# Performance work log

Hardware: AMD Instinct MI355X
Metric: run time of the kernel (lower is better)

The kernel has to match this reference:

```python
import jax, jax.numpy as jnp
import numpy as np

GRID = 32


def setup_inputs() -> dict:
    key = jax.random.key(0)
    k1, k2, k3 = jax.random.split(key, 3)
    # points in [-0.5, 0.5] per the module's asserts
    x = jax.random.uniform(k1, (8, 3, 50000), minval=-0.5, maxval=0.5, dtype=jnp.float32)
    # prep = Conv2d(3, 16, kernel_size=1): weight [C,3], bias [C]
    W = jax.random.normal(k2, (16, 3), dtype=jnp.float32) * 0.1
    bias = jax.random.normal(k3, (16,), dtype=jnp.float32) * 0.1
    return {"x": x, "W": W, "bias": bias}


def reference(x, W, bias):
    G = GRID
    b, _, n = x.shape
    reshaped = (x + 0.5) * G - 0.5                      # [b,3,n]
    ind1 = jnp.clip(jnp.floor(reshaped), 0.0, G - 1)
    ind2 = jnp.clip(jnp.ceil(reshaped), 0.0, G - 1)
    # 8 corners, ordered (floor/ceil over x, then y, then z) to match original list
    corners = []
    for cx in (ind1, ind2):
        for cy in (ind1, ind2):
            for cz in (ind1, ind2):
                corners.append(jnp.stack([cx[:, 0], cy[:, 1], cz[:, 2]], axis=1))
    ind = jnp.stack(corners, axis=-1)                   # [b,3,n,8]
    res = reshaped[..., None] - ind                     # [b,3,n,8] residuals
    flat_idx = (ind[:, 0] * (G * G) + ind[:, 1] * G + ind[:, 2]).astype(jnp.int32)  # [b,n,8]
    flat_idx = jnp.clip(flat_idx, 0, G ** 3)            # mirrors indices.clamp_(0, G**3)
    dist = jnp.linalg.norm(res, axis=1)                 # [b,n,8]
    weight = (dist < 0.87).astype(res.dtype)            # [b,n,8] (detached in original)
    # prep: 1x1 conv over channel dim
    feat = jnp.einsum('bknp,ck->bcnp', res, W) + bias[None, :, None, None]  # [b,c,n,8]
    feat = feat * weight[:, None]                       # mask by ball weight
    c = feat.shape[1]
    feat_f = feat.reshape(b, c, n * 8)
    w_f = jnp.broadcast_to(weight[:, None], feat.shape).reshape(b, c, n * 8)
    i_f = flat_idx.reshape(b, n * 8)

    def scatter_one(f, w, idx):
        g = jnp.zeros((c, G ** 3), f.dtype).at[:, idx].add(f)
        cnt = jnp.zeros((c, G ** 3), f.dtype).at[:, idx].add(w)
        return g, cnt

    grid, count = jax.vmap(scatter_one)(feat_f, w_f, i_f)  # [b,c,G^3] each
    grid = grid / jnp.maximum(count, 1.0)
    return grid.reshape(b, c, G, G, G)
```

## Files before the change

### kernel.cpp

```cpp
#include <hip/hip_runtime.h>

#define G 32
#define G2 (G*G)
#define G3 (G*G*G)
#define NPTS 50000
#define NB 8
#define NC 16
#define NCHUNK_PER_B 49
#define NCHUNK (NB*NCHUNK_PER_B)
#define SUBCAP 1024

#define OFF_HIST    0
#define OFF_PAYLOAD 65536


__global__ __launch_bounds__(1024) void ge_bin(const float* __restrict__ x,
                                               int* __restrict__ hist,
                                               unsigned long long* __restrict__ payload) {
    __shared__ unsigned long long sp[2048];
    __shared__ unsigned char spl[2048];
    __shared__ int h[G];
    __shared__ int offs[G + 1];

    const int tid = threadIdx.x;
    const int b   = blockIdx.y;
    const int c   = b * NCHUNK_PER_B + blockIdx.x;
    const int n   = blockIdx.x * 1024 + tid;
    const bool valid = n < NPTS;

    if (tid < G) h[tid] = 0;
    __syncthreads();

    unsigned long long e1 = 0, e2 = 0;
    int p1 = 0, p2 = 0, r1 = 0, r2 = 0;
    bool put1 = false, put2 = false;

    if (valid) {
        const float* xb = x + (size_t)b * 3 * NPTS;
        float rx = (xb[n]          + 0.5f) * 32.0f - 0.5f;
        float ry = (xb[NPTS + n]   + 0.5f) * 32.0f - 0.5f;
        float rz = (xb[2*NPTS + n] + 0.5f) * 32.0f - 0.5f;
        p1 = (int)fminf(fmaxf(floorf(rx), 0.0f), 31.0f);
        p2 = (int)fminf(fmaxf(ceilf (rx), 0.0f), 31.0f);

        float fy1 = fminf(fmaxf(floorf(ry), 0.0f), 31.0f);
        float fy2 = fminf(fmaxf(ceilf (ry), 0.0f), 31.0f);
        float fz1 = fminf(fmaxf(floorf(rz), 0.0f), 31.0f);
        float fz2 = fminf(fmaxf(ceilf (rz), 0.0f), 31.0f);
        float dy1 = ry - fy1, dy2 = ry - fy2;
        float dz1 = rz - fz1, dz2 = rz - fz2;
        float dy1s = dy1 * dy1, dy2s = dy2 * dy2;
        float dz1s = dz1 * dz1, dz2s = dz2 * dz2;

        int iy1 = (int)fy1, sy = (int)fy2 - iy1;
        int iz1 = (int)fz1, sz = (int)fz2 - iz1;
        int ay1 = (int)rintf(dy1 * 2048.0f) + 2048;
        int az1 = (int)rintf(dz1 * 2048.0f) + 2048;
        unsigned long long common =
              ((unsigned long long)(unsigned)ay1 << 30)
            | ((unsigned long long)(unsigned)az1 << 17)
            | ((unsigned long long)(unsigned)iy1 << 12)
            | ((unsigned long long)(unsigned)iz1 << 7)
            | ((unsigned long long)(unsigned)sy  << 6)
            | ((unsigned long long)(unsigned)sz  << 5);
        unsigned fr1 = (p1 == p2) ? 2u : 1u;

        {
            float dx = rx - (float)p1;
            float dx2 = dx * dx;
            float a0 = dx2 + dy1s, a1 = dx2 + dy2s;
            unsigned m = 0;
            if (a0 + dz1s < 0.7569f) m |= 1u;
            if (a0 + dz2s < 0.7569f) m |= 2u;
            if (a1 + dz1s < 0.7569f) m |= 4u;
            if (a1 + dz2s < 0.7569f) m |= 8u;
            if (m) {
                unsigned ax = (unsigned)((int)rintf(dx * 2048.0f) + 2048);
                e1 = ((unsigned long long)ax << 43) | common
                   | ((unsigned long long)(fr1 - 1u) << 4) | m;
                put1 = true;
                r1 = atomicAdd(&h[p1], 1);
            }
        }
        if (p2 != p1) {
            float dx = rx - (float)p2;
            float dx2 = dx * dx;
            float a0 = dx2 + dy1s, a1 = dx2 + dy2s;
            unsigned m = 0;
            if (a0 + dz1s < 0.7569f) m |= 1u;
            if (a0 + dz2s < 0.7569f) m |= 2u;
            if (a1 + dz1s < 0.7569f) m |= 4u;
            if (a1 + dz2s < 0.7569f) m |= 8u;
            if (m) {
                unsigned ax = (unsigned)((int)rintf(dx * 2048.0f) + 2048);
                e2 = ((unsigned long long)ax << 43) | common | m;
                put2 = true;
                r2 = atomicAdd(&h[p2], 1);
            }
        }
    }
    __syncthreads();

    if (tid == 0) {
        int run = 0;
        #pragma unroll
        for (int p = 0; p < G; ++p) { offs[p] = run; run += h[p]; }
        offs[G] = run;
    }
    __syncthreads();

    if (put1) {
        int i1 = offs[p1] + r1;
        sp[i1] = e1; spl[i1] = (unsigned char)p1;
    }
    if (put2) {
        int i2 = offs[p2] + r2;
        sp[i2] = e2; spl[i2] = (unsigned char)p2;
    }
    if (tid < G) hist[c * G + tid] = h[tid];
    __syncthreads();

    const int T = offs[G];
    unsigned long long* chunk_pl = payload + (size_t)c * G * SUBCAP;
    for (int e = tid; e < T; e += 1024) {
        int p = spl[e];
        chunk_pl[(size_t)p * SUBCAP + (e - offs[p])] = sp[e];
    }
}

__global__ __launch_bounds__(1024) void ge_accum(const unsigned long long* __restrict__ payload,
                                                 const int* __restrict__ hist,
                                                 const float* __restrict__ W,
                                                 const float* __restrict__ bias,
                                                 float* __restrict__ out) {
    __shared__ unsigned long long A[G2];
    const int tid = threadIdx.x;
    const int b = blockIdx.x >> 5;
    const int s = blockIdx.x & 31;

    A[tid] = 0ull;
    __syncthreads();

    const int wave = tid >> 6, lane = tid & 63;
    for (int blk = wave; blk < NCHUNK_PER_B; blk += 16) {
        const int cc = b * NCHUNK_PER_B + blk;
        const int ec = hist[cc * G + s];
        const unsigned long long* q = payload + ((size_t)cc * G + s) * SUBCAP;
        for (int i = lane; i < ec; i += 64) {
            unsigned long long e = q[i];
            unsigned m   = (unsigned)e & 15u;
            unsigned fr  = 1u + (((unsigned)e >> 4) & 1u);
            int sz  = ((int)e >> 5) & 1;
            int sy  = ((int)e >> 6) & 1;
            int iz1 = ((int)e >> 7) & 31;
            int iy1 = ((int)e >> 12) & 31;
            unsigned az1 = (unsigned)(e >> 17) & 0x1FFFu;
            unsigned ay1 = (unsigned)(e >> 30) & 0x1FFFu;
            unsigned ax  = (unsigned)(e >> 43) & 0x1FFFu;

            unsigned long long base = ((unsigned long long)fr << 57)
                                    | ((unsigned long long)(ax * fr) << 38);
            unsigned ayl = ay1 * fr, ayh = (ay1 - 2048u * sy) * fr;
            unsigned azl = az1 * fr, azh = (az1 - 2048u * sz) * fr;
            int cell = iy1 * G + iz1;

            if (m & 1u) atomicAdd(&A[cell],
                ((unsigned long long)ayl << 19) | azl | base);
            if (m & 2u) atomicAdd(&A[cell + sz],
                ((unsigned long long)ayl << 19) | azh | base);
            if (m & 4u) atomicAdd(&A[cell + G * sy],
                ((unsigned long long)ayh << 19) | azl | base);
            if (m & 8u) atomicAdd(&A[cell + G * sy + sz],
                ((unsigned long long)ayh << 19) | azh | base);
        }
    }
    __syncthreads();

    const unsigned long long a = A[tid];
    const float cw  = (float)(unsigned)(a >> 57);
    const float fxs = (float)(unsigned)((a >> 38) & 0x7FFFFull);
    const float fys = (float)(unsigned)((a >> 19) & 0x7FFFFull);
    const float fzs = (float)(unsigned)( a         & 0x7FFFFull);
    const float kq = 1.0f / 2048.0f;
    const float sx = (fxs - 2048.0f * cw) * kq;
    const float sy = (fys - 2048.0f * cw) * kq;
    const float sz = (fzs - 2048.0f * cw) * kq;
    const float inv = 1.0f / fmaxf(cw, 1.0f);

    float* ob = out + (size_t)b * NC * G3 + (size_t)s * G2 + tid;
    #pragma unroll
    for (int ch = 0; ch < NC; ++ch) {
        float v = W[ch * 3 + 0] * sx + W[ch * 3 + 1] * sy + W[ch * 3 + 2] * sz
                + cw * bias[ch];
        ob[(size_t)ch * G3] = v * inv;
    }
}

#define SEG 12288
#define QMAX SEG
__global__ __launch_bounds__(1024) void ge_fused(const float* __restrict__ x,
                                                 const float* __restrict__ W,
                                                 const float* __restrict__ bias,
                                                 float* __restrict__ out) {
    __shared__ float acc[G2][4];
    __shared__ int   q[QMAX];
    __shared__ int   qcount;
    const int b = blockIdx.x >> 5;
    const int s = blockIdx.x & 31;
    const float fs = (float)s;
    const int lane = threadIdx.x & 63;
    for (int i = threadIdx.x; i < G2 * 4; i += 1024) ((float*)acc)[i] = 0.0f;
    if (threadIdx.x == 0) qcount = 0;
    __syncthreads();
    const float* xb = x + (size_t)b * 3 * NPTS;
    for (int seg = 0; seg < NPTS; seg += SEG) {
        const int seg_end = (seg + SEG < NPTS) ? seg + SEG : NPTS;
        for (int base = seg; base < seg_end; base += 1024) {
            int n = base + threadIdx.x;
            bool pred = false; int tag = 0;
            if (n < seg_end) {
                float rx = (xb[n] + 0.5f) * 32.0f - 0.5f;
                int p1 = (int)fminf(fmaxf(floorf(rx), 0.0f), 31.0f);
                int p2 = (int)fminf(fmaxf(ceilf (rx), 0.0f), 31.0f);
                int reps = (p1 == s) + (p2 == s);
                pred = reps > 0;
                tag = n | (reps == 2 ? (int)0x80000000 : 0);
            }
            unsigned long long mask = __ballot(pred);
            int wcnt = __popcll(mask);
            if (wcnt) {
                int wbase = 0;
                if (lane == 0) wbase = atomicAdd(&qcount, wcnt);
                wbase = __shfl(wbase, 0);
                if (pred) q[wbase + __popcll(mask & ((1ULL << lane) - 1ULL))] = tag;
            }
        }
        __syncthreads();
        const int cnt = qcount;
        for (int i = threadIdx.x; i < cnt; i += 1024) {
            int e = q[i];
            int n = e & 0x7fffffff;
            float fr = (e < 0) ? 2.0f : 1.0f;
            float rx = (xb[n]          + 0.5f) * 32.0f - 0.5f;
            float ry = (xb[NPTS + n]   + 0.5f) * 32.0f - 0.5f;
            float rz = (xb[2*NPTS + n] + 0.5f) * 32.0f - 0.5f;
            float dx = rx - fs;
            float fy1 = fminf(fmaxf(floorf(ry), 0.0f), 31.0f);
            float fy2 = fminf(fmaxf(ceilf (ry), 0.0f), 31.0f);
            float fz1 = fminf(fmaxf(floorf(rz), 0.0f), 31.0f);
            float fz2 = fminf(fmaxf(ceilf (rz), 0.0f), 31.0f);
            #pragma unroll
            for (int cy = 0; cy < 2; ++cy) {
                float iy = cy ? fy2 : fy1;
                float dy = ry - iy;
                #pragma unroll
                for (int cz = 0; cz < 2; ++cz) {
                    float iz = cz ? fz2 : fz1;
                    float dz = rz - iz;
                    float d2 = dx * dx + dy * dy + dz * dz;
                    if (d2 < 0.7569f) {
                        int cell = (int)iy * G + (int)iz;
                        atomicAdd(&acc[cell][0], fr * dx);
                        atomicAdd(&acc[cell][1], fr * dy);
                        atomicAdd(&acc[cell][2], fr * dz);
                        atomicAdd(&acc[cell][3], fr);
                    }
                }
            }
        }
        __syncthreads();
        if (threadIdx.x == 0) qcount = 0;
        __syncthreads();
    }
    int cell = threadIdx.x;
    float sx = acc[cell][0], sy = acc[cell][1], sz = acc[cell][2], cnt = acc[cell][3];
    float inv = 1.0f / fmaxf(cnt, 1.0f);
    float* ob = out + (size_t)b * NC * G3 + (size_t)s * G2 + cell;
    #pragma unroll
    for (int c = 0; c < NC; ++c) {
        float v = W[c * 3 + 0] * sx + W[c * 3 + 1] * sy + W[c * 3 + 2] * sz
                + cnt * bias[c];
        ob[(size_t)c * G3] = v * inv;
    }
}

extern "C" void kernel_launch(void* const* d_in, const int* in_sizes, int n_in,
                              void* d_out, int out_size, void* d_ws, size_t ws_size,
                              hipStream_t stream) {
    const float* x    = (const float*)d_in[0];
    const float* W    = (const float*)d_in[1];
    const float* bias = (const float*)d_in[2];
    float* out = (float*)d_out;

    const size_t need = OFF_PAYLOAD
                      + (size_t)NCHUNK * G * SUBCAP * sizeof(unsigned long long);
    if (ws_size >= need) {
        char* wsb = (char*)d_ws;
        int* hist = (int*)(wsb + OFF_HIST);
        unsigned long long* payload = (unsigned long long*)(wsb + OFF_PAYLOAD);

        ge_bin  <<<dim3(NCHUNK_PER_B, NB), 1024, 0, stream>>>(x, hist, payload);
        ge_accum<<<NB * G, 1024, 0, stream>>>(payload, hist, W, bias, out);
    } else {
        ge_fused<<<NB * G, 1024, 0, stream>>>(x, W, bias, out);
    }
}
```

Baseline: 19.24 us.

## Compact per-bin payload via global atomic heads instead of per-chunk sub-buckets

Each binning block now reserves space in a single contiguous per-(batch, x-slice) bucket with one global atomicAdd per slice, replacing the per-chunk fixed-capacity sub-buckets and histogram. The accumulate kernel then streams one dense list per bin with all 1024 threads, instead of walking 49 sparse sub-lists per wave. Binning blocks shrink from 1024 to 256 threads to give more blocks. The change adds a memset launch and global atomics, and entries past a fixed capacity are silently dropped.

After: 25.52 us. 32.7% more time.

```diff
diff --git a/kernel.cpp b/kernel.cpp
--- a/kernel.cpp
+++ b/kernel.cpp
@@ -6,26 +6,26 @@
 #define NPTS 50000
 #define NB 8
 #define NC 16
-#define NCHUNK_PER_B 49
-#define NCHUNK (NB*NCHUNK_PER_B)
-#define SUBCAP 1024
-
-#define OFF_HIST    0
-#define OFF_PAYLOAD 65536
-
-
-__global__ __launch_bounds__(1024) void ge_bin(const float* __restrict__ x,
-                                               int* __restrict__ hist,
-                                               unsigned long long* __restrict__ payload) {
-    __shared__ unsigned long long sp[2048];
-    __shared__ unsigned char spl[2048];
+#define CHUNK 256
+#define NCHUNK_PER_B 196
+#define CAP 16384
+
+#define OFF_HEAD    0
+#define OFF_PAYLOAD 4096
+
+
+__global__ __launch_bounds__(256) void ge_bin(const float* __restrict__ x,
+                                              int* __restrict__ head,
+                                              unsigned long long* __restrict__ payload) {
+    __shared__ unsigned long long sp[2 * CHUNK];
+    __shared__ unsigned char spl[2 * CHUNK];
     __shared__ int h[G];
     __shared__ int offs[G + 1];
+    __shared__ int gbase[G];
 
     const int tid = threadIdx.x;
     const int b   = blockIdx.y;
-    const int c   = b * NCHUNK_PER_B + blockIdx.x;
-    const int n   = blockIdx.x * 1024 + tid;
+    const int n   = blockIdx.x * CHUNK + tid;
     const bool valid = n < NPTS;
 
     if (tid < G) h[tid] = 0;
@@ -109,70 +109,67 @@
     }
     __syncthreads();
 
-    if (put1) {
-        int i1 = offs[p1] + r1;
-        sp[i1] = e1; spl[i1] = (unsigned char)p1;
-    }
-    if (put2) {
-        int i2 = offs[p2] + r2;
-        sp[i2] = e2; spl[i2] = (unsigned char)p2;
-    }
-    if (tid < G) hist[c * G + tid] = h[tid];
+    if (tid < G) {
+        int c = h[tid];
+        gbase[tid] = c ? atomicAdd(&head[b * G + tid], c) : 0;
+    }
+    if (put1) { int i1 = offs[p1] + r1; sp[i1] = e1; spl[i1] = (unsigned char)p1; }
+    if (put2) { int i2 = offs[p2] + r2; sp[i2] = e2; spl[i2] = (unsigned char)p2; }
     __syncthreads();
 
     const int T = offs[G];
-    unsigned long long* chunk_pl = payload + (size_t)c * G * SUBCAP;
-    for (int e = tid; e < T; e += 1024) {
+    unsigned long long* pb = payload;
+    for (int e = tid; e < T; e += CHUNK) {
         int p = spl[e];
-        chunk_pl[(size_t)p * SUBCAP + (e - offs[p])] = sp[e];
+        size_t pos = (size_t)gbase[p] + (e - offs[p]);
+        if (pos < CAP)
+            pb[((size_t)b * G + p) * CAP + pos] = sp[e];
     }
 }
 
 __global__ __launch_bounds__(1024) void ge_accum(const unsigned long long* __restrict__ payload,
-                                                 const int* __restrict__ hist,
+                                                 const int* __restrict__ head,
                                                  const float* __restrict__ W,
                                                  const float* __restrict__ bias,
                                                  float* __restrict__ out) {
     __shared__ unsigned long long A[G2];
     const int tid = threadIdx.x;
-    const int b = blockIdx.x >> 5;
-    const int s = blockIdx.x & 31;
+    const int bin = blockIdx.x;
+    const int b = bin >> 5, s = bin & 31;
 
     A[tid] = 0ull;
     __syncthreads();
 
-    const int wave = tid >> 6, lane = tid & 63;
-    for (int blk = wave; blk < NCHUNK_PER_B; blk += 16) {
-        const int cc = b * NCHUNK_PER_B + blk;
-        const int ec = hist[cc * G + s];
-        const unsigned long long* q = payload + ((size_t)cc * G + s) * SUBCAP;
-        for (int i = lane; i < ec; i += 64) {
-            unsigned long long e = q[i];
-            unsigned m   = (unsigned)e & 15u;
-            unsigned fr  = 1u + (((unsigned)e >> 4) & 1u);
-            int sz  = ((int)e >> 5) & 1;
-            int sy  = ((int)e >> 6) & 1;
-            int iz1 = ((int)e >> 7) & 31;
-            int iy1 = ((int)e >> 12) & 31;
-            unsigned az1 = (unsigned)(e >> 17) & 0x1FFFu;
-            unsigned ay1 = (unsigned)(e >> 30) & 0x1FFFu;
-            unsigned ax  = (unsigned)(e >> 43) & 0x1FFFu;
-
-            unsigned long long base = ((unsigned long long)fr << 57)
-                                    | ((unsigned long long)(ax * fr) << 38);
-            unsigned ayl = ay1 * fr, ayh = (ay1 - 2048u * sy) * fr;
-            unsigned azl = az1 * fr, azh = (az1 - 2048u * sz) * fr;
-            int cell = iy1 * G + iz1;
-
-            if (m & 1u) atomicAdd(&A[cell],
-                ((unsigned long long)ayl << 19) | azl | base);
-            if (m & 2u) atomicAdd(&A[cell + sz],
-                ((unsigned long long)ayl << 19) | azh | base);
-            if (m & 4u) atomicAdd(&A[cell + G * sy],
-                ((unsigned long long)ayh << 19) | azl | base);
-            if (m & 8u) atomicAdd(&A[cell + G * sy + sz],
-                ((unsigned long long)ayh << 19) | azh | base);
-        }
+    int cnt = head[bin];
+    if (cnt > CAP) cnt = CAP;
+    const unsigned long long* q = payload + (size_t)bin * CAP;
+
+    for (int i = tid; i < cnt; i += 1024) {
+        unsigned long long e = q[i];
+        unsigned m   = (unsigned)e & 15u;
+        unsigned fr  = 1u + (((unsigned)e >> 4) & 1u);
+        int szi = ((int)e >> 5) & 1;
+        int syi = ((int)e >> 6) & 1;
+        int iz1 = ((int)e >> 7) & 31;
+        int iy1 = ((int)e >> 12) & 31;
+        unsigned az1 = (unsigned)(e >> 17) & 0x1FFFu;
+        unsigned ay1 = (unsigned)(e >> 30) & 0x1FFFu;
+        unsigned ax  = (unsigned)(e >> 43) & 0x1FFFu;
+
+        unsigned long long base = ((unsigned long long)fr << 57)
+                                | ((unsigned long long)(ax * fr) << 38);
+        unsigned ayl = ay1 * fr, ayh = (ay1 - 2048u * syi) * fr;
+        unsigned azl = az1 * fr, azh = (az1 - 2048u * szi) * fr;
+        int cell = iy1 * G + iz1;
+
+        if (m & 1u) atomicAdd(&A[cell],
+            ((unsigned long long)ayl << 19) | azl | base);
+        if (m & 2u) atomicAdd(&A[cell + szi],
+            ((unsigned long long)ayl << 19) | azh | base);
+        if (m & 4u) atomicAdd(&A[cell + G * syi],
+            ((unsigned long long)ayh << 19) | azl | base);
+        if (m & 8u) atomicAdd(&A[cell + G * syi + szi],
+            ((unsigned long long)ayh << 19) | azh | base);
     }
     __syncthreads();
 
@@ -292,15 +289,15 @@
     const float* bias = (const float*)d_in[2];
     float* out = (float*)d_out;
 
-    const size_t need = OFF_PAYLOAD
-                      + (size_t)NCHUNK * G * SUBCAP * sizeof(unsigned long long);
+    const size_t need = OFF_PAYLOAD + (size_t)NB * G * CAP * sizeof(unsigned long long);
     if (ws_size >= need) {
         char* wsb = (char*)d_ws;
-        int* hist = (int*)(wsb + OFF_HIST);
+        int* head = (int*)(wsb + OFF_HEAD);
         unsigned long long* payload = (unsigned long long*)(wsb + OFF_PAYLOAD);
 
-        ge_bin  <<<dim3(NCHUNK_PER_B, NB), 1024, 0, stream>>>(x, hist, payload);
-        ge_accum<<<NB * G, 1024, 0, stream>>>(payload, hist, W, bias, out);
+        hipMemsetAsync(head, 0, NB * G * sizeof(int), stream);
+        ge_bin  <<<dim3(NCHUNK_PER_B, NB), CHUNK, 0, stream>>>(x, head, payload);
+        ge_accum<<<NB * G, 1024, 0, stream>>>(payload, head, W, bias, out);
     } else {
         ge_fused<<<NB * G, 1024, 0, stream>>>(x, W, bias, out);
     }
```
